# Kernel tuning notes

Hardware: AMD Instinct MI355X
Metric: run time of the kernel (lower is better)

The kernel has to match this reference:

```python
import jax, jax.numpy as jnp
import numpy as np

N_NODES = 100000
N_EDGES = 800000
D = 64      # conv_dim == out_dim (skip connection)
H = 128     # conv hidden width


def _w(k, i, o):
    return jax.random.normal(k, (i, o), jnp.float32) * (1.0 / np.sqrt(i))


def setup_inputs() -> dict:
    key = jax.random.key(0)
    ks = jax.random.split(key, 40)
    inp = {
        "edge_feat": jax.random.normal(ks[0], (N_EDGES, D), jnp.float32),
        "node_feat": jax.random.normal(ks[1], (N_NODES, D), jnp.float32),
        "graph_attr": jax.random.normal(ks[2], (1, D), jnp.float32),
        "src": jax.random.randint(ks[3], (N_EDGES,), 0, N_NODES),
        "dst": jax.random.randint(ks[4], (N_EDGES,), 0, N_NODES),
        # pre-dense MLPs (dims=[64,64], Softplus, activate_last)
        "pre_edge_w": _w(ks[5], D, D), "pre_edge_b": jnp.zeros((D,), jnp.float32),
        "pre_node_w": _w(ks[6], D, D), "pre_node_b": jnp.zeros((D,), jnp.float32),
        "pre_attr_w": _w(ks[7], D, D), "pre_attr_b": jnp.zeros((D,), jnp.float32),
        # conv edge MLP: [4D, H, H, D]
        "edge_w0": _w(ks[8], 4 * D, H), "edge_b0": jnp.zeros((H,), jnp.float32),
        "edge_w1": _w(ks[9], H, H),     "edge_b1": jnp.zeros((H,), jnp.float32),
        "edge_w2": _w(ks[10], H, D),    "edge_b2": jnp.zeros((D,), jnp.float32),
        # conv node MLP: [3D, H, H, D]
        "node_w0": _w(ks[11], 3 * D, H), "node_b0": jnp.zeros((H,), jnp.float32),
        "node_w1": _w(ks[12], H, H),     "node_b1": jnp.zeros((H,), jnp.float32),
        "node_w2": _w(ks[13], H, D),     "node_b2": jnp.zeros((D,), jnp.float32),
        # conv attr MLP: [3D, H, H, D]
        "attr_w0": _w(ks[14], 3 * D, H), "attr_b0": jnp.zeros((H,), jnp.float32),
        "attr_w1": _w(ks[15], H, H),     "attr_b1": jnp.zeros((H,), jnp.float32),
        "attr_w2": _w(ks[16], H, D),     "attr_b2": jnp.zeros((D,), jnp.float32),
    }
    return inp


def _mlp(x, layers):
    # Linear + Softplus after every layer (activate_last=True)
    for w, b in layers:
        x = jax.nn.softplus(x @ w + b)
    return x


def reference(edge_feat, node_feat, graph_attr, src, dst,
              pre_edge_w, pre_edge_b, pre_node_w, pre_node_b, pre_attr_w, pre_attr_b,
              edge_w0, edge_b0, edge_w1, edge_b1, edge_w2, edge_b2,
              node_w0, node_b0, node_w1, node_b1, node_w2, node_b2,
              attr_w0, attr_b0, attr_w1, attr_b1, attr_w2, attr_b2):
    e_in, v_in, u_in = edge_feat, node_feat, graph_attr

    # pre-dense MLPs
    e = _mlp(edge_feat, [(pre_edge_w, pre_edge_b)])   # [E, D]
    v = _mlp(node_feat, [(pre_node_w, pre_node_b)])   # [N, D]
    u = _mlp(graph_attr, [(pre_attr_w, pre_attr_b)])  # [1, D]

    n_nodes = v.shape[0]

    # edge update: hstack([v_src, v_dst, e, u_broadcast]) -> edge MLP
    edge_in = jnp.concatenate(
        [v[src], v[dst], e, jnp.broadcast_to(u, (e.shape[0], u.shape[1]))], axis=1)  # [E, 4D]
    e_new = _mlp(edge_in, [(edge_w0, edge_b0), (edge_w1, edge_b1), (edge_w2, edge_b2)])  # [E, D]

    # node update: mean of incoming edge messages (segment-mean over dst)
    cnt = jax.ops.segment_sum(jnp.ones((e_new.shape[0], 1), e_new.dtype), dst,
                              num_segments=n_nodes)
    ve = jax.ops.segment_sum(e_new, dst, num_segments=n_nodes) / jnp.maximum(cnt, 1.0)
    node_in = jnp.concatenate(
        [v, ve, jnp.broadcast_to(u, (n_nodes, u.shape[1]))], axis=1)  # [N, 3D]
    v_new = _mlp(node_in, [(node_w0, node_b0), (node_w1, node_b1), (node_w2, node_b2)])  # [N, D]

    # attr update: mean readouts over edges and nodes
    ue = jnp.mean(e_new, axis=0, keepdims=True)  # [1, D]
    uv = jnp.mean(v_new, axis=0, keepdims=True)  # [1, D]
    attr_in = jnp.concatenate([u, ue, uv], axis=1)  # [1, 3D]
    u_new = _mlp(attr_in, [(attr_w0, attr_b0), (attr_w1, attr_b1), (attr_w2, attr_b2)])  # [1, D]

    # skip connections
    return (e_new + e_in, v_new + v_in, u_new + u_in)
```

## Files before the change

### kernel.cpp

```cpp
#include <hip/hip_runtime.h>
#include <cstddef>


typedef __attribute__((ext_vector_type(8))) short short8;
typedef __attribute__((ext_vector_type(4))) float f32x4;
typedef __attribute__((ext_vector_type(4))) unsigned int u32x4;
typedef __attribute__((ext_vector_type(2))) unsigned int u32x2;

__device__ __forceinline__ float sp(float x) {
    return fmaxf(x, 0.f) + __logf(1.f + __expf(-fabsf(x)));
}
__device__ __forceinline__ unsigned short f2bf(float x) {
    unsigned int u = __float_as_uint(x);
    u += 0x7fff + ((u >> 16) & 1);
    return (unsigned short)(u >> 16);
}
__device__ __forceinline__ unsigned int cvtpk(float lo, float hi) {
    unsigned int r;
    asm("v_cvt_pk_bf16_f32 %0, %1, %2" : "=v"(r) : "v"(lo), "v"(hi));
    return r;
}
__device__ __forceinline__ u32x4 pack8(f32x4 a, f32x4 b) {
    u32x4 r;
    r.x = cvtpk(a[0], a[1]); r.y = cvtpk(a[2], a[3]);
    r.z = cvtpk(b[0], b[1]); r.w = cvtpk(b[2], b[3]);
    return r;
}
__device__ __forceinline__ float bflo(unsigned int u) { return __uint_as_float(u << 16); }
__device__ __forceinline__ float bfhi(unsigned int u) { return __uint_as_float(u & 0xffff0000u); }
__device__ __forceinline__ int swz(int row, int chunk, int stride) {
    return row * stride + 128 * (chunk >> 3) + 16 * ((chunk & 7) ^ (row & 7));
}
__device__ __forceinline__ f32x4 mfma16(short8 a, short8 b, f32x4 c) {
    return __builtin_amdgcn_mfma_f32_16x16x32_bf16(a, b, c, 0, 0, 0);
}

__global__ __launch_bounds__(256) void wprep(
    const float* __restrict__ Wpe, const float* __restrict__ We0,
    const float* __restrict__ We1, const float* __restrict__ We2,
    const float* __restrict__ Wn0, const float* __restrict__ Wn1,
    const float* __restrict__ Wn2, const float* __restrict__ Wpn,
    unsigned short* __restrict__ out,
    const int* __restrict__ dst, int* __restrict__ cnt, int E)
{
    int idx = blockIdx.x * 256 + threadIdx.x;
    for (int i = idx; i < E; i += 384 * 256) atomicAdd(&cnt[dst[i]], 1);

    const float* src; int K, N, base;
    if      (idx < 4096)  { src = Wpe; K = 64;  N = 64;  base = 0; }
    else if (idx < 28672) { src = We0; K = 192; N = 128; base = 4096; }
    else if (idx < 45056) { src = We1; K = 128; N = 128; base = 28672; }
    else if (idx < 53248) { src = We2; K = 128; N = 64;  base = 45056; }
    else if (idx < 69632) { src = Wn0; K = 128; N = 128; base = 53248; }
    else if (idx < 86016) { src = Wn1; K = 128; N = 128; base = 69632; }
    else if (idx < 94208) { src = Wn2; K = 128; N = 64;  base = 86016; }
    else if (idx < 98304) { src = Wpn; K = 64;  N = 64;  base = 94208; }
    else return;
    int r = idx - base, n = r / K, k = r % K;
    out[idx] = f2bf(src[(size_t)k * N + n]);
}

__global__ __launch_bounds__(256) void pre_node_kernel(
    const float* __restrict__ nf, const unsigned short* __restrict__ WpnT,
    const float* __restrict__ b, unsigned short* __restrict__ vb, int N)
{
    __shared__ __align__(16) char lds[16384];
    const int t = threadIdx.x, w = t >> 6, l = t & 63;
    const int l15 = l & 15, l4 = l >> 4;
    const int n0 = blockIdx.x * 64;

#pragma unroll
    for (int rr = 0; rr < 2; ++rr) {
        int f = t + 256 * rr;
        int e = f >> 3, c = f & 7;
        int n = n0 + e; if (n >= N) n = N - 1;
        const float* p = nf + (size_t)n * 64 + c * 8;
        f32x4 x0 = *(const f32x4*)p, x1 = *(const f32x4*)(p + 4);
        *(u32x4*)(lds + swz(e, c, 128)) = pack8(x0, x1);
    }
    __syncthreads();
    {
        const int nr = w * 16;
        short8 A0 = *(const short8*)(WpnT + (nr + l15) * 64 + l4 * 8);
        short8 A1 = *(const short8*)(WpnT + (nr + l15) * 64 + 32 + l4 * 8);
        f32x4 bb = *(const f32x4*)(b + nr + l4 * 4);
        const int ochunk = (nr >> 3) + (l4 >> 1), obyte = (l4 & 1) * 8;
#pragma unroll
        for (int tt = 0; tt < 4; ++tt) {
            short8 b0 = *(const short8*)(lds + swz(tt * 16 + l15, l4, 128));
            short8 b1 = *(const short8*)(lds + swz(tt * 16 + l15, 4 + l4, 128));
            f32x4 acc = {0.f, 0.f, 0.f, 0.f};
            acc = mfma16(A0, b0, acc);
            acc = mfma16(A1, b1, acc);
            u32x2 p;
            p.x = cvtpk(sp(acc[0] + bb[0]), sp(acc[1] + bb[1]));
            p.y = cvtpk(sp(acc[2] + bb[2]), sp(acc[3] + bb[3]));
            *(u32x2*)(lds + 8192 + swz(tt * 16 + l15, ochunk, 128) + obyte) = p;
        }
    }
    __syncthreads();
#pragma unroll
    for (int rr = 0; rr < 2; ++rr) {
        int f = t + 256 * rr;
        int e = f >> 3, c = f & 7;
        int n = n0 + e;
        if (n < N) {
            u32x4 d = *(const u32x4*)(lds + 8192 + swz(e, c, 128));
            *(u32x4*)(vb + (size_t)n * 64 + c * 8) = d;
        }
    }
}

__global__ void pre_attr_kernel(
    const float* __restrict__ ga, const float* __restrict__ Wpa, const float* __restrict__ bpa,
    const float* __restrict__ eW0, const float* __restrict__ eb0,
    const float* __restrict__ nW0, const float* __restrict__ nb0,
    float* __restrict__ u, float* __restrict__ c0e, float* __restrict__ c0n)
{
    __shared__ float us[64];
    const int t = threadIdx.x;
    if (t < 64) {
        float acc = bpa[t];
        for (int k = 0; k < 64; ++k) acc += ga[k] * Wpa[k * 64 + t];
        float uu = sp(acc);
        us[t] = uu;
        u[t] = uu;
    }
    __syncthreads();
    if (t < 128) {
        float acc = eb0[t];
        for (int k = 0; k < 64; ++k) acc += us[k] * eW0[(192 + k) * 128 + t];
        c0e[t] = acc;
        float accn = nb0[t];
        for (int k = 0; k < 64; ++k) accn += us[k] * nW0[(128 + k) * 128 + t];
        c0n[t] = accn;
    }
}

__global__ __launch_bounds__(256) void scan1_kernel(
    const int* __restrict__ cnt, int* __restrict__ woff, int* __restrict__ bsum, int N)
{
    __shared__ int wsum[4];
    const int t = threadIdx.x, lane = t & 63, wv = t >> 6;
    const int i0 = blockIdx.x * 1024 + t * 4;
    int v0 = (i0 + 0 < N) ? cnt[i0 + 0] : 0;
    int v1 = (i0 + 1 < N) ? cnt[i0 + 1] : 0;
    int v2 = (i0 + 2 < N) ? cnt[i0 + 2] : 0;
    int v3 = (i0 + 3 < N) ? cnt[i0 + 3] : 0;
    int ts = v0 + v1 + v2 + v3;
    int sc = ts;
    for (int d = 1; d < 64; d <<= 1) {
        int up = __shfl_up(sc, d);
        if (lane >= d) sc += up;
    }
    if (lane == 63) wsum[wv] = sc;
    __syncthreads();
    int woffs = 0;
    for (int i = 0; i < wv; ++i) woffs += wsum[i];
    int ex = woffs + sc - ts;
    if (i0 + 0 < N) woff[i0 + 0] = ex;            ex += v0;
    if (i0 + 1 < N) woff[i0 + 1] = ex;            ex += v1;
    if (i0 + 2 < N) woff[i0 + 2] = ex;            ex += v2;
    if (i0 + 3 < N) woff[i0 + 3] = ex;
    if (t == 0) bsum[blockIdx.x] = wsum[0] + wsum[1] + wsum[2] + wsum[3];
}

__global__ void scan2_kernel(int* __restrict__ bsum, int nb)
{
    __shared__ int s[256];
    const int t = threadIdx.x;
    if (t < nb) s[t] = bsum[t];
    __syncthreads();
    if (t == 0) {
        int a = 0;
        for (int i = 0; i < nb; ++i) { int v = s[i]; s[i] = a; a += v; }
    }
    __syncthreads();
    if (t < nb) bsum[t] = s[t];
}

__global__ __launch_bounds__(256) void scan3_kernel(
    int* __restrict__ woff, int* __restrict__ wcur, const int* __restrict__ bsum, int N)
{
    const int base = blockIdx.x * 1024;
    const int add = bsum[blockIdx.x];
#pragma unroll
    for (int r = 0; r < 4; ++r) {
        int i = base + r * 256 + threadIdx.x;
        if (i < N) {
            int o = woff[i] + add;
            woff[i] = o;
            wcur[i] = o;
        }
    }
}

__global__ __launch_bounds__(256) void scatter_kernel(
    const int* __restrict__ dst, int* __restrict__ wcur,
    int* __restrict__ eidx, int* __restrict__ slot, int E)
{
    int i = blockIdx.x * 256 + threadIdx.x;
    if (i < E) {
        int d = dst[i];
        int p = atomicAdd(&wcur[d], 1);
        eidx[p] = i;
        slot[i] = p;
    }
}

#define ELDS_X  0
#define ELDS_H  24576
#define ELDS_EF 40960

__global__ __launch_bounds__(256, 3) void edge_kernel(
    const float* __restrict__ ef, const unsigned short* __restrict__ vb,
    const int* __restrict__ src, const int* __restrict__ dst,
    const int* __restrict__ slot,
    const unsigned short* __restrict__ WpeT, const float* __restrict__ bpe,
    const unsigned short* __restrict__ W0T, const float* __restrict__ c0e,
    const unsigned short* __restrict__ W1T, const float* __restrict__ b1,
    const unsigned short* __restrict__ W2T, const float* __restrict__ b2,
    float* __restrict__ e_out, unsigned short* __restrict__ ebf)
{
    __shared__ __align__(16) char lds[49152];
    const int t = threadIdx.x;
    const int w = t >> 6, l = t & 63;
    const int l15 = l & 15, l4 = l >> 4;
    const int e0 = blockIdx.x * 64;

#pragma unroll
    for (int rr = 0; rr < 4; ++rr) {
        int f = t + 256 * rr;
        int e = f >> 4, c = f & 15;
        int node = (c < 8) ? src[e0 + e] : dst[e0 + e];
        u32x4 d = *(const u32x4*)(vb + (size_t)node * 64 + (c & 7) * 8);
        *(u32x4*)(lds + ELDS_X + swz(e, c, 384)) = d;
    }
    f32x4 efr[4];
    int sl[4];
#pragma unroll
    for (int rr = 0; rr < 4; ++rr) {
        int f = t + 256 * rr;
        int e = f >> 4, c = f & 15;
        sl[rr] = slot[e0 + e];
        efr[rr] = *(const f32x4*)(ef + (size_t)(e0 + e) * 64 + c * 4);
        u32x2 p;
        p.x = cvtpk(efr[rr][0], efr[rr][1]);
        p.y = cvtpk(efr[rr][2], efr[rr][3]);
        *(u32x2*)(lds + ELDS_EF + swz(e, c >> 1, 128) + (c & 1) * 8) = p;
    }
    const int nrS = w * 16;
    const int nr0 = w * 32, nr1 = nr0 + 16;
    short8 Wp[2], W0f[2][6], W1f[2][4], W2f[4];
    Wp[0] = *(const short8*)(WpeT + (nrS + l15) * 64 + l4 * 8);
    Wp[1] = *(const short8*)(WpeT + (nrS + l15) * 64 + 32 + l4 * 8);
#pragma unroll
    for (int a = 0; a < 2; ++a)
#pragma unroll
        for (int ks = 0; ks < 6; ++ks)
            W0f[a][ks] = *(const short8*)(W0T + (nr0 + a * 16 + l15) * 192 + ks * 32 + l4 * 8);
#pragma unroll
    for (int a = 0; a < 2; ++a)
#pragma unroll
        for (int ks = 0; ks < 4; ++ks)
            W1f[a][ks] = *(const short8*)(W1T + (nr0 + a * 16 + l15) * 128 + ks * 32 + l4 * 8);
#pragma unroll
    for (int ks = 0; ks < 4; ++ks)
        W2f[ks] = *(const short8*)(W2T + (nrS + l15) * 128 + ks * 32 + l4 * 8);
    __syncthreads();

    {
        f32x4 bb = *(const f32x4*)(bpe + nrS + l4 * 4);
        const int ochunk = ((128 + nrS) >> 3) + (l4 >> 1), obyte = (l4 & 1) * 8;
#pragma unroll
        for (int tt = 0; tt < 4; ++tt) {
            short8 b0 = *(const short8*)(lds + ELDS_EF + swz(tt * 16 + l15, l4, 128));
            short8 b1 = *(const short8*)(lds + ELDS_EF + swz(tt * 16 + l15, 4 + l4, 128));
            f32x4 acc = {0.f, 0.f, 0.f, 0.f};
            acc = mfma16(Wp[0], b0, acc);
            acc = mfma16(Wp[1], b1, acc);
            u32x2 p;
            p.x = cvtpk(sp(acc[0] + bb[0]), sp(acc[1] + bb[1]));
            p.y = cvtpk(sp(acc[2] + bb[2]), sp(acc[3] + bb[3]));
            *(u32x2*)(lds + ELDS_X + swz(tt * 16 + l15, ochunk, 384) + obyte) = p;
        }
    }
    __syncthreads();

    {
        f32x4 bb0 = *(const f32x4*)(c0e + nr0 + l4 * 4);
        f32x4 bb1 = *(const f32x4*)(c0e + nr1 + l4 * 4);
        const int oc0 = (nr0 >> 3) + (l4 >> 1), oc1 = (nr1 >> 3) + (l4 >> 1);
        const int obyte = (l4 & 1) * 8;
#pragma unroll
        for (int tt = 0; tt < 4; ++tt) {
            f32x4 a0 = {0.f, 0.f, 0.f, 0.f}, a1 = {0.f, 0.f, 0.f, 0.f};
#pragma unroll
            for (int ks = 0; ks < 6; ++ks) {
                short8 b = *(const short8*)(lds + ELDS_X + swz(tt * 16 + l15, ks * 4 + l4, 384));
                a0 = mfma16(W0f[0][ks], b, a0);
                a1 = mfma16(W0f[1][ks], b, a1);
            }
            u32x2 p0, p1;
            p0.x = cvtpk(sp(a0[0] + bb0[0]), sp(a0[1] + bb0[1]));
            p0.y = cvtpk(sp(a0[2] + bb0[2]), sp(a0[3] + bb0[3]));
            p1.x = cvtpk(sp(a1[0] + bb1[0]), sp(a1[1] + bb1[1]));
            p1.y = cvtpk(sp(a1[2] + bb1[2]), sp(a1[3] + bb1[3]));
            *(u32x2*)(lds + ELDS_H + swz(tt * 16 + l15, oc0, 256) + obyte) = p0;
            *(u32x2*)(lds + ELDS_H + swz(tt * 16 + l15, oc1, 256) + obyte) = p1;
        }
    }
    __syncthreads();

    {
        f32x4 bb0 = *(const f32x4*)(b1 + nr0 + l4 * 4);
        f32x4 bb1 = *(const f32x4*)(b1 + nr1 + l4 * 4);
        const int oc0 = (nr0 >> 3) + (l4 >> 1), oc1 = (nr1 >> 3) + (l4 >> 1);
        const int obyte = (l4 & 1) * 8;
#pragma unroll
        for (int tt = 0; tt < 4; ++tt) {
            f32x4 a0 = {0.f, 0.f, 0.f, 0.f}, a1 = {0.f, 0.f, 0.f, 0.f};
#pragma unroll
            for (int ks = 0; ks < 4; ++ks) {
                short8 b = *(const short8*)(lds + ELDS_H + swz(tt * 16 + l15, ks * 4 + l4, 256));
                a0 = mfma16(W1f[0][ks], b, a0);
                a1 = mfma16(W1f[1][ks], b, a1);
            }
            u32x2 p0, p1;
            p0.x = cvtpk(sp(a0[0] + bb0[0]), sp(a0[1] + bb0[1]));
            p0.y = cvtpk(sp(a0[2] + bb0[2]), sp(a0[3] + bb0[3]));
            p1.x = cvtpk(sp(a1[0] + bb1[0]), sp(a1[1] + bb1[1]));
            p1.y = cvtpk(sp(a1[2] + bb1[2]), sp(a1[3] + bb1[3]));
            *(u32x2*)(lds + ELDS_X + swz(tt * 16 + l15, oc0, 256) + obyte) = p0;
            *(u32x2*)(lds + ELDS_X + swz(tt * 16 + l15, oc1, 256) + obyte) = p1;
        }
    }
    __syncthreads();

    {
        f32x4 bb = *(const f32x4*)(b2 + nrS + l4 * 4);
        const int ochunk = (nrS >> 2) + l4;
#pragma unroll
        for (int tt = 0; tt < 4; ++tt) {
            f32x4 acc = {0.f, 0.f, 0.f, 0.f};
#pragma unroll
            for (int ks = 0; ks < 4; ++ks) {
                short8 b = *(const short8*)(lds + ELDS_X + swz(tt * 16 + l15, ks * 4 + l4, 256));
                acc = mfma16(W2f[ks], b, acc);
            }
            f32x4 y = {sp(acc[0] + bb[0]), sp(acc[1] + bb[1]),
                       sp(acc[2] + bb[2]), sp(acc[3] + bb[3])};
            *(f32x4*)(lds + ELDS_H + swz(tt * 16 + l15, ochunk, 256)) = y;
        }
    }
    __syncthreads();

#pragma unroll
    for (int rr = 0; rr < 4; ++rr) {
        int f = t + 256 * rr;
        int e = f >> 4, c = f & 15;
        f32x4 en = *(const f32x4*)(lds + ELDS_H + swz(e, c, 256));
        f32x4 o = en + efr[rr];
        __builtin_nontemporal_store(o, (f32x4*)(e_out + (size_t)(e0 + e) * 64 + c * 4));
        if (ebf) {
            u32x2 pk;
            pk.x = cvtpk(en[0], en[1]);
            pk.y = cvtpk(en[2], en[3]);
            *(u32x2*)(ebf + (size_t)sl[rr] * 64 + c * 4) = pk;
        }
    }
}

#define NLDS_X 0
#define NLDS_H 16384

__global__ __launch_bounds__(256, 3) void node_kernel(
    const float* __restrict__ nf, const unsigned short* __restrict__ vb,
    const int* __restrict__ cnt, const int* __restrict__ woff,
    const int* __restrict__ eidx,
    const unsigned short* __restrict__ ebf,
    const float* __restrict__ e_out_full, const float* __restrict__ ef_full,
    const unsigned short* __restrict__ W0T, const float* __restrict__ c0n,
    const unsigned short* __restrict__ W1T, const float* __restrict__ b1,
    const unsigned short* __restrict__ W2T, const float* __restrict__ b2,
    float* __restrict__ v_out, float* __restrict__ acc_e, float* __restrict__ acc_v,
    int N)
{
    __shared__ __align__(16) char lds[32768];
    const int t = threadIdx.x;
    const int w = t >> 6, l = t & 63;
    const int l15 = l & 15, l4 = l >> 4;
    const int n0 = blockIdx.x * 64;

#pragma unroll
    for (int rr = 0; rr < 2; ++rr) {
        int f = t + 256 * rr;
        int e = f >> 3, c = f & 7;
        int n = n0 + e; if (n >= N) n = N - 1;
        u32x4 d = *(const u32x4*)(vb + (size_t)n * 64 + c * 8);
        *(u32x4*)(lds + NLDS_X + swz(e, c, 256)) = d;
    }
    {
        const int e = t >> 2, p = t & 3;
        const int n = n0 + e;
        const bool valid = n < N;
        f32x4 a0 = {0,0,0,0}, a1 = {0,0,0,0}, a2 = {0,0,0,0}, a3 = {0,0,0,0};
        float rc = 0.f;
        if (valid) {
            const int off = woff[n], deg = cnt[n];
            rc = 1.f / fmaxf((float)deg, 1.f);
            if (ebf) {
                const unsigned short* base = ebf + (size_t)off * 64 + p * 16;
                for (int j = 0; j < deg; ++j) {
                    u32x4 qa = *(const u32x4*)(base);
                    u32x4 qb = *(const u32x4*)(base + 8);
                    base += 64;
                    a0[0] += bflo(qa.x); a0[1] += bfhi(qa.x);
                    a0[2] += bflo(qa.y); a0[3] += bfhi(qa.y);
                    a1[0] += bflo(qa.z); a1[1] += bfhi(qa.z);
                    a1[2] += bflo(qa.w); a1[3] += bfhi(qa.w);
                    a2[0] += bflo(qb.x); a2[1] += bfhi(qb.x);
                    a2[2] += bflo(qb.y); a2[3] += bfhi(qb.y);
                    a3[0] += bflo(qb.z); a3[1] += bfhi(qb.z);
                    a3[2] += bflo(qb.w); a3[3] += bfhi(qb.w);
                }
            } else {
                for (int j = 0; j < deg; ++j) {
                    int ed = eidx[off + j];
                    const float* ro = e_out_full + (size_t)ed * 64 + p * 16;
                    const float* ri = ef_full + (size_t)ed * 64 + p * 16;
                    a0 += *(const f32x4*)(ro + 0)  - *(const f32x4*)(ri + 0);
                    a1 += *(const f32x4*)(ro + 4)  - *(const f32x4*)(ri + 4);
                    a2 += *(const f32x4*)(ro + 8)  - *(const f32x4*)(ri + 8);
                    a3 += *(const f32x4*)(ro + 12) - *(const f32x4*)(ri + 12);
                }
            }
        }
        *(f32x4*)(lds + NLDS_H + swz(e, p * 4 + 0, 256)) = a0;
        *(f32x4*)(lds + NLDS_H + swz(e, p * 4 + 1, 256)) = a1;
        *(f32x4*)(lds + NLDS_H + swz(e, p * 4 + 2, 256)) = a2;
        *(f32x4*)(lds + NLDS_H + swz(e, p * 4 + 3, 256)) = a3;
        *(u32x4*)(lds + NLDS_X + swz(e, 8 + 2 * p, 256)) = pack8(a0 * rc, a1 * rc);
        *(u32x4*)(lds + NLDS_X + swz(e, 9 + 2 * p, 256)) = pack8(a2 * rc, a3 * rc);
    }
    __syncthreads();
    if (t < 64) {
        float s = 0.f;
        for (int row = 0; row < 64; ++row)
            s += *(const float*)(lds + NLDS_H + swz(row, t >> 2, 256) + (t & 3) * 4);
        atomicAdd(acc_e + t, s);
    }
    __syncthreads();

    {
        const int nr0 = w * 32, nr1 = nr0 + 16;
        short8 A[2][4];
#pragma unroll
        for (int a = 0; a < 2; ++a)
#pragma unroll
            for (int ks = 0; ks < 4; ++ks)
                A[a][ks] = *(const short8*)(W0T + (nr0 + a * 16 + l15) * 128 + ks * 32 + l4 * 8);
        f32x4 bb0 = *(const f32x4*)(c0n + nr0 + l4 * 4);
        f32x4 bb1 = *(const f32x4*)(c0n + nr1 + l4 * 4);
        const int oc0 = (nr0 >> 3) + (l4 >> 1), oc1 = (nr1 >> 3) + (l4 >> 1);
        const int obyte = (l4 & 1) * 8;
#pragma unroll
        for (int tt = 0; tt < 4; ++tt) {
            f32x4 a0 = {0.f, 0.f, 0.f, 0.f}, a1 = {0.f, 0.f, 0.f, 0.f};
#pragma unroll
            for (int ks = 0; ks < 4; ++ks) {
                short8 b = *(const short8*)(lds + NLDS_X + swz(tt * 16 + l15, ks * 4 + l4, 256));
                a0 = mfma16(A[0][ks], b, a0);
                a1 = mfma16(A[1][ks], b, a1);
            }
            u32x2 p0, p1;
            p0.x = cvtpk(sp(a0[0] + bb0[0]), sp(a0[1] + bb0[1]));
            p0.y = cvtpk(sp(a0[2] + bb0[2]), sp(a0[3] + bb0[3]));
            p1.x = cvtpk(sp(a1[0] + bb1[0]), sp(a1[1] + bb1[1]));
            p1.y = cvtpk(sp(a1[2] + bb1[2]), sp(a1[3] + bb1[3]));
            *(u32x2*)(lds + NLDS_H + swz(tt * 16 + l15, oc0, 256) + obyte) = p0;
            *(u32x2*)(lds + NLDS_H + swz(tt * 16 + l15, oc1, 256) + obyte) = p1;
        }
    }
    __syncthreads();

    {
        const int nr0 = w * 32, nr1 = nr0 + 16;
        short8 A[2][4];
#pragma unroll
        for (int a = 0; a < 2; ++a)
#pragma unroll
            for (int ks = 0; ks < 4; ++ks)
                A[a][ks] = *(const short8*)(W1T + (nr0 + a * 16 + l15) * 128 + ks * 32 + l4 * 8);
        f32x4 bb0 = *(const f32x4*)(b1 + nr0 + l4 * 4);
        f32x4 bb1 = *(const f32x4*)(b1 + nr1 + l4 * 4);
        const int oc0 = (nr0 >> 3) + (l4 >> 1), oc1 = (nr1 >> 3) + (l4 >> 1);
        const int obyte = (l4 & 1) * 8;
#pragma unroll
        for (int tt = 0; tt < 4; ++tt) {
            f32x4 a0 = {0.f, 0.f, 0.f, 0.f}, a1 = {0.f, 0.f, 0.f, 0.f};
#pragma unroll
            for (int ks = 0; ks < 4; ++ks) {
                short8 b = *(const short8*)(lds + NLDS_H + swz(tt * 16 + l15, ks * 4 + l4, 256));
                a0 = mfma16(A[0][ks], b, a0);
                a1 = mfma16(A[1][ks], b, a1);
            }
            u32x2 p0, p1;
            p0.x = cvtpk(sp(a0[0] + bb0[0]), sp(a0[1] + bb0[1]));
            p0.y = cvtpk(sp(a0[2] + bb0[2]), sp(a0[3] + bb0[3]));
            p1.x = cvtpk(sp(a1[0] + bb1[0]), sp(a1[1] + bb1[1]));
            p1.y = cvtpk(sp(a1[2] + bb1[2]), sp(a1[3] + bb1[3]));
            *(u32x2*)(lds + NLDS_X + swz(tt * 16 + l15, oc0, 256) + obyte) = p0;
            *(u32x2*)(lds + NLDS_X + swz(tt * 16 + l15, oc1, 256) + obyte) = p1;
        }
    }
    __syncthreads();

    {
        const int nr = w * 16;
        short8 A[4];
#pragma unroll
        for (int ks = 0; ks < 4; ++ks)
            A[ks] = *(const short8*)(W2T + (nr + l15) * 128 + ks * 32 + l4 * 8);
        f32x4 bb = *(const f32x4*)(b2 + nr + l4 * 4);
        const int ochunk = (nr >> 2) + l4;
#pragma unroll
        for (int tt = 0; tt < 4; ++tt) {
            f32x4 acc = {0.f, 0.f, 0.f, 0.f};
#pragma unroll
            for (int ks = 0; ks < 4; ++ks) {
                short8 b = *(const short8*)(lds + NLDS_X + swz(tt * 16 + l15, ks * 4 + l4, 256));
                acc = mfma16(A[ks], b, acc);
            }
            bool valid = (n0 + tt * 16 + l15) < N;
            f32x4 y;
            y[0] = valid ? sp(acc[0] + bb[0]) : 0.f;
            y[1] = valid ? sp(acc[1] + bb[1]) : 0.f;
            y[2] = valid ? sp(acc[2] + bb[2]) : 0.f;
            y[3] = valid ? sp(acc[3] + bb[3]) : 0.f;
            *(f32x4*)(lds + NLDS_H + swz(tt * 16 + l15, ochunk, 256)) = y;
        }
    }
    __syncthreads();

#pragma unroll
    for (int rr = 0; rr < 4; ++rr) {
        int f = t + 256 * rr;
        int e = f >> 4, c = f & 15;
        int n = n0 + e;
        if (n < N) {
            f32x4 vn = *(const f32x4*)(lds + NLDS_H + swz(e, c, 256));
            f32x4 x = *(const f32x4*)(nf + (size_t)n * 64 + c * 4);
            f32x4 o = vn + x;
            __builtin_nontemporal_store(o, (f32x4*)(v_out + (size_t)n * 64 + c * 4));
        }
    }
    if (t < 64) {
        float s = 0.f;
        for (int row = 0; row < 64; ++row)
            s += *(const float*)(lds + NLDS_H + swz(row, t >> 2, 256) + (t & 3) * 4);
        atomicAdd(acc_v + t, s);
    }
}

__global__ void attr_kernel(
    const float* __restrict__ ga, const float* __restrict__ u,
    const float* __restrict__ acc_e, const float* __restrict__ acc_v,
    const float* __restrict__ W0, const float* __restrict__ b0,
    const float* __restrict__ W1, const float* __restrict__ b1,
    const float* __restrict__ W2, const float* __restrict__ b2,
    float* __restrict__ out_u, float Einv, float Ninv)
{
    __shared__ float ain[192];
    __shared__ float h0[128];
    __shared__ float h1[128];
    const int t = threadIdx.x;
    if (t < 64) {
        ain[t] = u[t];
        ain[64 + t] = acc_e[t] * Einv;
        ain[128 + t] = acc_v[t] * Ninv;
    }
    __syncthreads();
    if (t < 128) {
        float a = b0[t];
        for (int k = 0; k < 192; ++k) a += ain[k] * W0[k * 128 + t];
        h0[t] = sp(a);
    }
    __syncthreads();
    if (t < 128) {
        float a = b1[t];
        for (int k = 0; k < 128; ++k) a += h0[k] * W1[k * 128 + t];
        h1[t] = sp(a);
    }
    __syncthreads();
    if (t < 64) {
        float a = b2[t];
        for (int k = 0; k < 128; ++k) a += h1[k] * W2[k * 64 + t];
        out_u[t] = sp(a) + ga[t];
    }
}

extern "C" void kernel_launch(void* const* d_in, const int* in_sizes, int n_in,
                              void* d_out, int out_size, void* d_ws, size_t ws_size,
                              hipStream_t stream)
{
    const float* edge_feat = (const float*)d_in[0];
    const float* node_feat = (const float*)d_in[1];
    const float* graph_attr = (const float*)d_in[2];
    const int*   src = (const int*)d_in[3];
    const int*   dst = (const int*)d_in[4];
    const float* pre_edge_w = (const float*)d_in[5];
    const float* pre_edge_b = (const float*)d_in[6];
    const float* pre_node_w = (const float*)d_in[7];
    const float* pre_node_b = (const float*)d_in[8];
    const float* pre_attr_w = (const float*)d_in[9];
    const float* pre_attr_b = (const float*)d_in[10];
    const float* edge_w0 = (const float*)d_in[11];
    const float* edge_b0 = (const float*)d_in[12];
    const float* edge_w1 = (const float*)d_in[13];
    const float* edge_b1 = (const float*)d_in[14];
    const float* edge_w2 = (const float*)d_in[15];
    const float* edge_b2 = (const float*)d_in[16];
    const float* node_w0 = (const float*)d_in[17];
    const float* node_b0 = (const float*)d_in[18];
    const float* node_w1 = (const float*)d_in[19];
    const float* node_b1 = (const float*)d_in[20];
    const float* node_w2 = (const float*)d_in[21];
    const float* node_b2 = (const float*)d_in[22];
    const float* attr_w0 = (const float*)d_in[23];
    const float* attr_b0 = (const float*)d_in[24];
    const float* attr_w1 = (const float*)d_in[25];
    const float* attr_b1 = (const float*)d_in[26];
    const float* attr_w2 = (const float*)d_in[27];
    const float* attr_b2 = (const float*)d_in[28];

    const int E = in_sizes[0] / 64;
    const int N = in_sizes[1] / 64;
    const int NB = (N + 1023) / 1024;

    char* wsB = (char*)d_ws;
    size_t off = 0;
    auto alloc = [&](size_t bytes) { char* p = wsB + off; off += (bytes + 15) & ~(size_t)15; return p; };
    float* acc_e = (float*)alloc(64 * 4);
    float* acc_v = (float*)alloc(64 * 4);
    int*   cnt   = (int*)alloc((size_t)N * 4);
    float* u     = (float*)alloc(64 * 4);
    float* c0e   = (float*)alloc(128 * 4);
    float* c0n   = (float*)alloc(128 * 4);
    int*   bsum  = (int*)alloc((size_t)NB * 4);
    int*   woff  = (int*)alloc((size_t)N * 4);
    int*   wcur  = (int*)alloc((size_t)N * 4);
    int*   eidx  = (int*)alloc((size_t)E * 4);
    int*   slot  = (int*)alloc((size_t)E * 4);
    unsigned short* wT = (unsigned short*)alloc((size_t)98304 * 2);
    unsigned short* vb = (unsigned short*)alloc((size_t)N * 64 * 2);
    size_t off_no_ebf = off;
    unsigned short* ebf = (unsigned short*)alloc((size_t)E * 64 * 2);
    const bool use_ebf = (off <= ws_size);
    if (!use_ebf) { ebf = nullptr; off = off_no_ebf; }

    unsigned short* WpeT = wT;
    unsigned short* We0T = wT + 4096;
    unsigned short* We1T = wT + 28672;
    unsigned short* We2T = wT + 45056;
    unsigned short* Wn0T = wT + 53248;
    unsigned short* Wn1T = wT + 69632;
    unsigned short* Wn2T = wT + 86016;
    unsigned short* WpnT = wT + 94208;

    float* e_out = (float*)d_out;
    float* v_out = e_out + (size_t)E * 64;
    float* u_out = v_out + (size_t)N * 64;

    hipMemsetAsync(acc_e, 0, (size_t)(128 + N) * 4, stream);

    wprep<<<384, 256, 0, stream>>>(pre_edge_w, edge_w0, edge_w1, edge_w2,
                                   node_w0, node_w1, node_w2, pre_node_w, wT,
                                   dst, cnt, E);
    pre_node_kernel<<<(N + 63) / 64, 256, 0, stream>>>(node_feat, WpnT, pre_node_b, vb, N);
    pre_attr_kernel<<<1, 128, 0, stream>>>(graph_attr, pre_attr_w, pre_attr_b,
                                           edge_w0, edge_b0, node_w0, node_b0,
                                           u, c0e, c0n);
    scan1_kernel<<<NB, 256, 0, stream>>>(cnt, woff, bsum, N);
    scan2_kernel<<<1, 256, 0, stream>>>(bsum, NB);
    scan3_kernel<<<NB, 256, 0, stream>>>(woff, wcur, bsum, N);
    scatter_kernel<<<(E + 255) / 256, 256, 0, stream>>>(dst, wcur, eidx, slot, E);
    edge_kernel<<<E / 64, 256, 0, stream>>>(
        edge_feat, vb, src, dst, slot,
        WpeT, pre_edge_b, We0T, c0e, We1T, edge_b1, We2T, edge_b2,
        e_out, ebf);
    node_kernel<<<(N + 63) / 64, 256, 0, stream>>>(
        node_feat, vb, cnt, woff, eidx, ebf, e_out, edge_feat,
        Wn0T, c0n, Wn1T, node_b1, Wn2T, node_b2,
        v_out, acc_e, acc_v, N);
    attr_kernel<<<1, 128, 0, stream>>>(
        graph_attr, u, acc_e, acc_v,
        attr_w0, attr_b0, attr_w1, attr_b1, attr_w2, attr_b2,
        u_out, 1.f / (float)E, 1.f / (float)N);
}
```

Before: 520.8 us.

## Split edge kernel work across eight waves per block

The edge MLP kernel now runs 512 threads (8 waves) per 64-edge block instead of 256. Each wave holds weight fragments for 16 output rows instead of 32, and the 64-wide layers split the edge tiles between wave halves, so per-thread register pressure drops. The aim is more resident waves to hide gather latency for node features. The cost is more threads sharing the same LDS tile and barriers, with each wave doing less MFMA work per sync.

Result: slower. 565.2 us (+8.5%).

```diff
diff --git a/kernel.cpp b/kernel.cpp
--- a/kernel.cpp
+++ b/kernel.cpp
@@ -212,7 +212,7 @@
 #define ELDS_H  24576
 #define ELDS_EF 40960
 
-__global__ __launch_bounds__(256, 3) void edge_kernel(
+__global__ __launch_bounds__(512, 4) void edge_kernel(
     const float* __restrict__ ef, const unsigned short* __restrict__ vb,
     const int* __restrict__ src, const int* __restrict__ dst,
     const int* __restrict__ slot,
@@ -229,18 +229,18 @@
     const int e0 = blockIdx.x * 64;
 
 #pragma unroll
-    for (int rr = 0; rr < 4; ++rr) {
-        int f = t + 256 * rr;
+    for (int rr = 0; rr < 2; ++rr) {
+        int f = t + 512 * rr;
         int e = f >> 4, c = f & 15;
         int node = (c < 8) ? src[e0 + e] : dst[e0 + e];
         u32x4 d = *(const u32x4*)(vb + (size_t)node * 64 + (c & 7) * 8);
         *(u32x4*)(lds + ELDS_X + swz(e, c, 384)) = d;
     }
-    f32x4 efr[4];
-    int sl[4];
-#pragma unroll
-    for (int rr = 0; rr < 4; ++rr) {
-        int f = t + 256 * rr;
+    f32x4 efr[2];
+    int sl[2];
+#pragma unroll
+    for (int rr = 0; rr < 2; ++rr) {
+        int f = t + 512 * rr;
         int e = f >> 4, c = f & 15;
         sl[rr] = slot[e0 + e];
         efr[rr] = *(const f32x4*)(ef + (size_t)(e0 + e) * 64 + c * 4);
@@ -249,31 +249,29 @@
         p.y = cvtpk(efr[rr][2], efr[rr][3]);
         *(u32x2*)(lds + ELDS_EF + swz(e, c >> 1, 128) + (c & 1) * 8) = p;
     }
-    const int nrS = w * 16;
-    const int nr0 = w * 32, nr1 = nr0 + 16;
-    short8 Wp[2], W0f[2][6], W1f[2][4], W2f[4];
-    Wp[0] = *(const short8*)(WpeT + (nrS + l15) * 64 + l4 * 8);
-    Wp[1] = *(const short8*)(WpeT + (nrS + l15) * 64 + 32 + l4 * 8);
-#pragma unroll
-    for (int a = 0; a < 2; ++a)
-#pragma unroll
-        for (int ks = 0; ks < 6; ++ks)
-            W0f[a][ks] = *(const short8*)(W0T + (nr0 + a * 16 + l15) * 192 + ks * 32 + l4 * 8);
-#pragma unroll
-    for (int a = 0; a < 2; ++a)
-#pragma unroll
-        for (int ks = 0; ks < 4; ++ks)
-            W1f[a][ks] = *(const short8*)(W1T + (nr0 + a * 16 + l15) * 128 + ks * 32 + l4 * 8);
+    const int nrQ = (w & 3) * 16;
+    const int hQ  = w >> 2;
+    const int nr  = w * 16;
+    short8 Wp[2], W0f[6], W1f[4], W2f[4];
+    Wp[0] = *(const short8*)(WpeT + (nrQ + l15) * 64 + l4 * 8);
+    Wp[1] = *(const short8*)(WpeT + (nrQ + l15) * 64 + 32 + l4 * 8);
+#pragma unroll
+    for (int ks = 0; ks < 6; ++ks)
+        W0f[ks] = *(const short8*)(W0T + (nr + l15) * 192 + ks * 32 + l4 * 8);
 #pragma unroll
     for (int ks = 0; ks < 4; ++ks)
-        W2f[ks] = *(const short8*)(W2T + (nrS + l15) * 128 + ks * 32 + l4 * 8);
-    __syncthreads();
-
-    {
-        f32x4 bb = *(const f32x4*)(bpe + nrS + l4 * 4);
-        const int ochunk = ((128 + nrS) >> 3) + (l4 >> 1), obyte = (l4 & 1) * 8;
-#pragma unroll
-        for (int tt = 0; tt < 4; ++tt) {
+        W1f[ks] = *(const short8*)(W1T + (nr + l15) * 128 + ks * 32 + l4 * 8);
+#pragma unroll
+    for (int ks = 0; ks < 4; ++ks)
+        W2f[ks] = *(const short8*)(W2T + (nrQ + l15) * 128 + ks * 32 + l4 * 8);
+    __syncthreads();
+
+    {
+        f32x4 bb = *(const f32x4*)(bpe + nrQ + l4 * 4);
+        const int ochunk = ((128 + nrQ) >> 3) + (l4 >> 1), obyte = (l4 & 1) * 8;
+#pragma unroll
+        for (int th = 0; th < 2; ++th) {
+            int tt = hQ * 2 + th;
             short8 b0 = *(const short8*)(lds + ELDS_EF + swz(tt * 16 + l15, l4, 128));
             short8 b1 = *(const short8*)(lds + ELDS_EF + swz(tt * 16 + l15, 4 + l4, 128));
             f32x4 acc = {0.f, 0.f, 0.f, 0.f};
@@ -288,60 +286,49 @@
     __syncthreads();
 
     {
-        f32x4 bb0 = *(const f32x4*)(c0e + nr0 + l4 * 4);
-        f32x4 bb1 = *(const f32x4*)(c0e + nr1 + l4 * 4);
-        const int oc0 = (nr0 >> 3) + (l4 >> 1), oc1 = (nr1 >> 3) + (l4 >> 1);
-        const int obyte = (l4 & 1) * 8;
+        f32x4 bb = *(const f32x4*)(c0e + nr + l4 * 4);
+        const int oc = (nr >> 3) + (l4 >> 1), obyte = (l4 & 1) * 8;
 #pragma unroll
         for (int tt = 0; tt < 4; ++tt) {
-            f32x4 a0 = {0.f, 0.f, 0.f, 0.f}, a1 = {0.f, 0.f, 0.f, 0.f};
+            f32x4 a0 = {0.f, 0.f, 0.f, 0.f};
 #pragma unroll
             for (int ks = 0; ks < 6; ++ks) {
                 short8 b = *(const short8*)(lds + ELDS_X + swz(tt * 16 + l15, ks * 4 + l4, 384));
-                a0 = mfma16(W0f[0][ks], b, a0);
-                a1 = mfma16(W0f[1][ks], b, a1);
+                a0 = mfma16(W0f[ks], b, a0);
             }
-            u32x2 p0, p1;
-            p0.x = cvtpk(sp(a0[0] + bb0[0]), sp(a0[1] + bb0[1]));
-            p0.y = cvtpk(sp(a0[2] + bb0[2]), sp(a0[3] + bb0[3]));
-            p1.x = cvtpk(sp(a1[0] + bb1[0]), sp(a1[1] + bb1[1]));
-            p1.y = cvtpk(sp(a1[2] + bb1[2]), sp(a1[3] + bb1[3]));
-            *(u32x2*)(lds + ELDS_H + swz(tt * 16 + l15, oc0, 256) + obyte) = p0;
-            *(u32x2*)(lds + ELDS_H + swz(tt * 16 + l15, oc1, 256) + obyte) = p1;
-        }
-    }
-    __syncthreads();
-
-    {
-        f32x4 bb0 = *(const f32x4*)(b1 + nr0 + l4 * 4);
-        f32x4 bb1 = *(const f32x4*)(b1 + nr1 + l4 * 4);
-        const int oc0 = (nr0 >> 3) + (l4 >> 1), oc1 = (nr1 >> 3) + (l4 >> 1);
-        const int obyte = (l4 & 1) * 8;
+            u32x2 p;
+            p.x = cvtpk(sp(a0[0] + bb[0]), sp(a0[1] + bb[1]));
+            p.y = cvtpk(sp(a0[2] + bb[2]), sp(a0[3] + bb[3]));
+            *(u32x2*)(lds + ELDS_H + swz(tt * 16 + l15, oc, 256) + obyte) = p;
+        }
+    }
+    __syncthreads();
+
+    {
+        f32x4 bb = *(const f32x4*)(b1 + nr + l4 * 4);
+        const int oc = (nr >> 3) + (l4 >> 1), obyte = (l4 & 1) * 8;
 #pragma unroll
         for (int tt = 0; tt < 4; ++tt) {
-            f32x4 a0 = {0.f, 0.f, 0.f, 0.f}, a1 = {0.f, 0.f, 0.f, 0.f};
+            f32x4 a0 = {0.f, 0.f, 0.f, 0.f};
 #pragma unroll
             for (int ks = 0; ks < 4; ++ks) {
                 short8 b = *(const short8*)(lds + ELDS_H + swz(tt * 16 + l15, ks * 4 + l4, 256));
-                a0 = mfma16(W1f[0][ks], b, a0);
-                a1 = mfma16(W1f[1][ks], b, a1);
+                a0 = mfma16(W1f[ks], b, a0);
             }
-            u32x2 p0, p1;
-            p0.x = cvtpk(sp(a0[0] + bb0[0]), sp(a0[1] + bb0[1]));
-            p0.y = cvtpk(sp(a0[2] + bb0[2]), sp(a0[3] + bb0[3]));
-            p1.x = cvtpk(sp(a1[0] + bb1[0]), sp(a1[1] + bb1[1]));
-            p1.y = cvtpk(sp(a1[2] + bb1[2]), sp(a1[3] + bb1[3]));
-            *(u32x2*)(lds + ELDS_X + swz(tt * 16 + l15, oc0, 256) + obyte) = p0;
-            *(u32x2*)(lds + ELDS_X + swz(tt * 16 + l15, oc1, 256) + obyte) = p1;
-        }
-    }
-    __syncthreads();
-
-    {
-        f32x4 bb = *(const f32x4*)(b2 + nrS + l4 * 4);
-        const int ochunk = (nrS >> 2) + l4;
-#pragma unroll
-        for (int tt = 0; tt < 4; ++tt) {
+            u32x2 p;
+            p.x = cvtpk(sp(a0[0] + bb[0]), sp(a0[1] + bb[1]));
+            p.y = cvtpk(sp(a0[2] + bb[2]), sp(a0[3] + bb[3]));
+            *(u32x2*)(lds + ELDS_X + swz(tt * 16 + l15, oc, 256) + obyte) = p;
+        }
+    }
+    __syncthreads();
+
+    {
+        f32x4 bb = *(const f32x4*)(b2 + nrQ + l4 * 4);
+        const int ochunk = (nrQ >> 2) + l4;
+#pragma unroll
+        for (int th = 0; th < 2; ++th) {
+            int tt = hQ * 2 + th;
             f32x4 acc = {0.f, 0.f, 0.f, 0.f};
 #pragma unroll
             for (int ks = 0; ks < 4; ++ks) {
@@ -356,8 +343,8 @@
     __syncthreads();
 
 #pragma unroll
-    for (int rr = 0; rr < 4; ++rr) {
-        int f = t + 256 * rr;
+    for (int rr = 0; rr < 2; ++rr) {
+        int f = t + 512 * rr;
         int e = f >> 4, c = f & 15;
         f32x4 en = *(const f32x4*)(lds + ELDS_H + swz(e, c, 256));
         f32x4 o = en + efr[rr];
@@ -685,7 +672,7 @@
     scan2_kernel<<<1, 256, 0, stream>>>(bsum, NB);
     scan3_kernel<<<NB, 256, 0, stream>>>(woff, wcur, bsum, N);
     scatter_kernel<<<(E + 255) / 256, 256, 0, stream>>>(dst, wcur, eidx, slot, E);
-    edge_kernel<<<E / 64, 256, 0, stream>>>(
+    edge_kernel<<<E / 64, 512, 0, stream>>>(
         edge_feat, vb, src, dst, slot,
         WpeT, pre_edge_b, We0T, c0e, We1T, edge_b1, We2T, edge_b2,
         e_out, ebf);
```
